# Kernel tuning notes

Hardware: AMD Instinct MI355X
Metric: run time of the kernel (lower is better)

The kernel has to match this reference:

```python
import jax, jax.numpy as jnp
import numpy as np
import math

D_MODEL = 512
N_HEADS = 8
MAX_SEQ_LEN = 4096
DENSITY = 0.3


def _make_random_mask(key, seq_len, density=DENSITY):
    # rand < density, symmetrized via (m + m.T)/2, clamped to [0,1], diag = 1
    u = jax.random.uniform(key, (seq_len, seq_len), dtype=jnp.float32)
    m = (u < density).astype(jnp.float32)
    m = jnp.clip((m + m.T) * 0.5, 0.0, 1.0)
    return m.at[jnp.diag_indices(seq_len)].set(1.0)


def setup_inputs() -> dict:
    key = jax.random.key(0)
    ks = jax.random.split(key, 10)
    B, T, C = 2, 4096, D_MODEL
    scale = 1.0 / math.sqrt(C)
    x = jax.random.normal(ks[0], (B, T, C), dtype=jnp.float32)
    mask = _make_random_mask(ks[1], MAX_SEQ_LEN)[:T, :T]
    # Linear weights stored as (in, out): y = x @ W + b
    Wq = jax.random.normal(ks[2], (C, C), dtype=jnp.float32) * scale
    Wk = jax.random.normal(ks[3], (C, C), dtype=jnp.float32) * scale
    Wv = jax.random.normal(ks[4], (C, C), dtype=jnp.float32) * scale
    Wo = jax.random.normal(ks[5], (C, C), dtype=jnp.float32) * scale
    bq = jax.random.normal(ks[6], (C,), dtype=jnp.float32) * scale
    bk = jax.random.normal(ks[7], (C,), dtype=jnp.float32) * scale
    bv = jax.random.normal(ks[8], (C,), dtype=jnp.float32) * scale
    bo = jax.random.normal(ks[9], (C,), dtype=jnp.float32) * scale
    return {"x": x, "mask": mask, "Wq": Wq, "bq": bq, "Wk": Wk, "bk": bk,
            "Wv": Wv, "bv": bv, "Wo": Wo, "bo": bo}


def reference(x, mask, Wq, bq, Wk, bk, Wv, bv, Wo, bo):
    B, T, C = x.shape
    H = N_HEADS
    dk = C // H
    q = (x @ Wq + bq).reshape(B, T, H, dk)
    k = (x @ Wk + bk).reshape(B, T, H, dk)
    v = (x @ Wv + bv).reshape(B, T, H, dk)
    # scores: [B, H, T, T]
    attn = jnp.einsum('bthd,bshd->bhts', q, k) / math.sqrt(dk)
    attn = attn * mask[None, None, :, :]  # multiplicative mask PRE-softmax
    p = jax.nn.softmax(attn, axis=-1)
    out = jnp.einsum('bhts,bshd->bthd', p, v).reshape(B, T, C)
    return out @ Wo + bo
```

## Files before the change

kernel.cpp:

```cpp
#include <hip/hip_runtime.h>
#include <math.h>

#define D_MODEL 512
#define N_HEADS 8
#define DK 64
#define QSCALE (0.0625f * 1.44269504089f)

typedef __attribute__((ext_vector_type(8))) short short8;
typedef __attribute__((ext_vector_type(4))) float f32x4;
typedef __attribute__((ext_vector_type(16))) float f32x16;

typedef __attribute__((address_space(1))) const unsigned as1_uint;
typedef __attribute__((address_space(3))) unsigned as3_uint;

__device__ __forceinline__ unsigned short f2bf(float f) {
    unsigned u = __builtin_bit_cast(unsigned, f);
    u = (u + 0x7fff + ((u >> 16) & 1)) >> 16;
    return (unsigned short)u;
}

__global__ __launch_bounds__(256) void cvt_x_kernel(const float* __restrict__ x,
                                                    unsigned short* __restrict__ xb, int n8)
{
    int i = blockIdx.x * 256 + threadIdx.x;
    if (i >= n8) return;
    float4 a = ((const float4*)x)[i * 2];
    float4 b = ((const float4*)x)[i * 2 + 1];
    short8 o;
    o[0] = f2bf(a.x); o[1] = f2bf(a.y); o[2] = f2bf(a.z); o[3] = f2bf(a.w);
    o[4] = f2bf(b.x); o[5] = f2bf(b.y); o[6] = f2bf(b.z); o[7] = f2bf(b.w);
    ((short8*)xb)[i] = o;
}

__global__ __launch_bounds__(256) void cvt_mask_kernel(const float* __restrict__ m,
                                                       unsigned char* __restrict__ mu, int n4)
{
    int i = blockIdx.x * 256 + threadIdx.x;
    if (i >= n4) return;
    float4 v = ((const float4*)m)[i];
    uchar4 o = { (unsigned char)(v.x * 2.0f + 0.5f),
                 (unsigned char)(v.y * 2.0f + 0.5f),
                 (unsigned char)(v.z * 2.0f + 0.5f),
                 (unsigned char)(v.w * 2.0f + 0.5f) };
    ((uchar4*)mu)[i] = o;
}

__global__ __launch_bounds__(256) void cvt_wt_kernel(const float* __restrict__ W,
                                                     unsigned short* __restrict__ Wt)
{
    __shared__ float tile[64][65];
    int t = threadIdx.x;
    int c0 = blockIdx.x * 64;
    int r0 = blockIdx.y * 64;
    #pragma unroll
    for (int i = 0; i < 16; i++) {
        int e = i * 256 + t, r = e >> 6, c = e & 63;
        tile[c][r] = W[(size_t)(r0 + r) * D_MODEL + c0 + c];
    }
    __syncthreads();
    #pragma unroll
    for (int i = 0; i < 16; i++) {
        int e = i * 256 + t, n = e >> 6, kk = e & 63;
        Wt[(size_t)(c0 + n) * D_MODEL + r0 + kk] = f2bf(tile[n][kk]);
    }
}

__global__ __launch_bounds__(512) void gemm_qkv_kernel(
    const unsigned short* __restrict__ A, const unsigned short* __restrict__ Wt,
    const float* __restrict__ bq, const float* __restrict__ bk, const float* __restrict__ bv,
    unsigned short* __restrict__ qb, unsigned short* __restrict__ kb,
    unsigned short* __restrict__ vb, int M, int T)
{
    constexpr int K = D_MODEL;
    __shared__ unsigned short As[2][128 * 32];
    __shared__ unsigned short Bs[2][128 * 32];
    int t = threadIdx.x;
    int lane = t & 63, w = t >> 6;
    int ql = lane & 15, kg = lane >> 4;
    int m0 = blockIdx.y * 128, n0 = blockIdx.x * 128;
    int wm = w >> 2, wn = w & 3;
    bool vmode = (n0 >= 1024);

    const unsigned short* srcA = A + (size_t)(m0 + (t >> 2)) * K + (t & 3) * 8;
    const unsigned short* srcB = Wt + (size_t)(n0 + (t >> 2)) * K + (t & 3) * 8;

    f32x4 acc[4][2];
    #pragma unroll
    for (int i = 0; i < 4; i++)
        #pragma unroll
        for (int j = 0; j < 2; j++) { f32x4 z = {0.f, 0.f, 0.f, 0.f}; acc[i][j] = z; }

    constexpr int NIT = K / 32;
    int cur = 0;
    __builtin_amdgcn_global_load_lds((as1_uint*)(srcA),
        (as3_uint*)((char*)&As[0][0] + w * 1024), 16, 0, 0);
    __builtin_amdgcn_global_load_lds((as1_uint*)(srcB),
        (as3_uint*)((char*)&Bs[0][0] + w * 1024), 16, 0, 0);
    __syncthreads();

    for (int it = 0; it < NIT; ++it) {
        if (it + 1 < NIT) {
            int k0 = (it + 1) * 32;
            __builtin_amdgcn_global_load_lds((as1_uint*)(srcA + k0),
                (as3_uint*)((char*)&As[cur ^ 1][0] + w * 1024), 16, 0, 0);
            __builtin_amdgcn_global_load_lds((as1_uint*)(srcB + k0),
                (as3_uint*)((char*)&Bs[cur ^ 1][0] + w * 1024), 16, 0, 0);
        }
        short8 af[4], bfr[2];
        #pragma unroll
        for (int fm = 0; fm < 4; fm++)
            af[fm] = *(const short8*)((const char*)&As[cur][0] + (wm * 64 + fm * 16 + ql) * 64 + kg * 16);
        #pragma unroll
        for (int fn = 0; fn < 2; fn++)
            bfr[fn] = *(const short8*)((const char*)&Bs[cur][0] + (wn * 32 + fn * 16 + ql) * 64 + kg * 16);
        if (vmode) {
            #pragma unroll
            for (int fm = 0; fm < 4; fm++)
                #pragma unroll
                for (int fn = 0; fn < 2; fn++)
                    acc[fm][fn] = __builtin_amdgcn_mfma_f32_16x16x32_bf16(bfr[fn], af[fm], acc[fm][fn], 0, 0, 0);
        } else {
            #pragma unroll
            for (int fm = 0; fm < 4; fm++)
                #pragma unroll
                for (int fn = 0; fn < 2; fn++)
                    acc[fm][fn] = __builtin_amdgcn_mfma_f32_16x16x32_bf16(af[fm], bfr[fn], acc[fm][fn], 0, 0, 0);
        }
        __syncthreads();
        cur ^= 1;
    }

    #pragma unroll
    for (int fm = 0; fm < 4; fm++) {
        #pragma unroll
        for (int fn = 0; fn < 2; fn++) {
            if (vmode) {
                int m = m0 + wm * 64 + fm * 16 + ql;
                int b = m / T, tt = m % T;
                #pragma unroll
                for (int r = 0; r < 4; r++) {
                    int n = (n0 - 1024) + wn * 32 + fn * 16 + kg * 4 + r;
                    float val = acc[fm][fn][r] + bv[n];
                    int h = n >> 6, d = n & 63;
                    vb[((size_t)(b * N_HEADS + h) * DK + d) * T + tt] = f2bf(val);
                }
            } else {
                int n = n0 + wn * 32 + fn * 16 + ql;
                int nn = n & 511;
                bool isq = (n0 < 512);
                float bn = isq ? bq[nn] : bk[nn];
                unsigned short* dst = isq ? qb : kb;
                int h = nn >> 6, d = nn & 63;
                #pragma unroll
                for (int r = 0; r < 4; r++) {
                    int m = m0 + wm * 64 + fm * 16 + kg * 4 + r;
                    int b = m / T, tt = m % T;
                    float val = acc[fm][fn][r] + bn;
                    if (isq) val *= QSCALE;
                    dst[((size_t)(b * N_HEADS + h) * T + tt) * DK + d] = f2bf(val);
                }
            }
        }
    }
}

__global__ __launch_bounds__(512) void gemm_out_kernel(
    const unsigned short* __restrict__ A, const unsigned short* __restrict__ Bt,
    const float* __restrict__ bias, float* __restrict__ outp, int M)
{
    constexpr int K = D_MODEL;
    __shared__ unsigned short As[2][128 * 32];
    __shared__ unsigned short Bs[2][128 * 32];
    int t = threadIdx.x;
    int lane = t & 63, w = t >> 6;
    int ql = lane & 15, kg = lane >> 4;
    int m0 = blockIdx.y * 128, n0 = blockIdx.x * 128;
    int wm = w >> 2, wn = w & 3;

    const unsigned short* srcA = A + (size_t)(m0 + (t >> 2)) * K + (t & 3) * 8;
    const unsigned short* srcB = Bt + (size_t)(n0 + (t >> 2)) * K + (t & 3) * 8;

    f32x4 acc[4][2];
    #pragma unroll
    for (int i = 0; i < 4; i++)
        #pragma unroll
        for (int j = 0; j < 2; j++) { f32x4 z = {0.f, 0.f, 0.f, 0.f}; acc[i][j] = z; }

    constexpr int NIT = K / 32;
    int cur = 0;
    __builtin_amdgcn_global_load_lds((as1_uint*)(srcA),
        (as3_uint*)((char*)&As[0][0] + w * 1024), 16, 0, 0);
    __builtin_amdgcn_global_load_lds((as1_uint*)(srcB),
        (as3_uint*)((char*)&Bs[0][0] + w * 1024), 16, 0, 0);
    __syncthreads();

    for (int it = 0; it < NIT; ++it) {
        if (it + 1 < NIT) {
            int k0 = (it + 1) * 32;
            __builtin_amdgcn_global_load_lds((as1_uint*)(srcA + k0),
                (as3_uint*)((char*)&As[cur ^ 1][0] + w * 1024), 16, 0, 0);
            __builtin_amdgcn_global_load_lds((as1_uint*)(srcB + k0),
                (as3_uint*)((char*)&Bs[cur ^ 1][0] + w * 1024), 16, 0, 0);
        }
        short8 af[4], bfr[2];
        #pragma unroll
        for (int fm = 0; fm < 4; fm++)
            af[fm] = *(const short8*)((const char*)&As[cur][0] + (wm * 64 + fm * 16 + ql) * 64 + kg * 16);
        #pragma unroll
        for (int fn = 0; fn < 2; fn++)
            bfr[fn] = *(const short8*)((const char*)&Bs[cur][0] + (wn * 32 + fn * 16 + ql) * 64 + kg * 16);
        #pragma unroll
        for (int fm = 0; fm < 4; fm++)
            #pragma unroll
            for (int fn = 0; fn < 2; fn++)
                acc[fm][fn] = __builtin_amdgcn_mfma_f32_16x16x32_bf16(af[fm], bfr[fn], acc[fm][fn], 0, 0, 0);
        __syncthreads();
        cur ^= 1;
    }

    #pragma unroll
    for (int fm = 0; fm < 4; fm++) {
        #pragma unroll
        for (int fn = 0; fn < 2; fn++) {
            int n = n0 + wn * 32 + fn * 16 + ql;
            float bn = bias[n];
            #pragma unroll
            for (int r = 0; r < 4; r++) {
                int m = m0 + wm * 64 + fm * 16 + kg * 4 + r;
                outp[(size_t)m * D_MODEL + n] = acc[fm][fn][r] + bn;
            }
        }
    }
}

__global__ __launch_bounds__(256) void attn_mfma_kernel(
    const unsigned short* __restrict__ q, const unsigned short* __restrict__ k,
    const unsigned short* __restrict__ v, const unsigned char* __restrict__ mu,
    unsigned short* __restrict__ out, int B, int T)
{
    __shared__ unsigned short Ks[2][64 * 64];
    __shared__ unsigned short Vt[2][64 * 64];

    int t = threadIdx.x;
    int lane = t & 63, w = t >> 6;
    int ln = lane & 31, hi = lane >> 5;
    int bh = blockIdx.x;
    int qt = blockIdx.y;
    int hh = bh & (N_HEADS - 1), b = bh >> 3;
    int qr0 = qt * 128;

    const char* kbase = (const char*)(k + (size_t)bh * T * DK);
    const char* vbase = (const char*)(v + (size_t)bh * DK * T);

    int lin0 = w * 1024 + lane * 16;
    int lin1 = 4096 + lin0;
    int row0 = lin0 >> 7, row1 = lin1 >> 7;
    int sw0 = (row0 & 7) << 4, sw1 = (row1 & 7) << 4;
    const char* gK0 = kbase + (lin0 ^ sw0);
    const char* gK1 = kbase + (lin1 ^ sw1);
    const char* gV0 = vbase + (size_t)row0 * (2 * T) + ((lin0 & 127) ^ sw0);
    const char* gV1 = vbase + (size_t)row1 * (2 * T) + ((lin1 & 127) ^ sw1);

    short8 qfr[4];
    {
        const unsigned short* qrow = q + ((size_t)bh * T + qr0 + w * 32 + ln) * DK + hi * 8;
        #pragma unroll
        for (int ks = 0; ks < 4; ks++)
            qfr[ks] = *(const short8*)(qrow + ks * 16);
    }

    const unsigned char* mbase = mu + (size_t)(qr0 + w * 32 + ln) * T + 4 * hi;

    f32x16 oacc[2];
    #pragma unroll
    for (int db = 0; db < 2; db++)
        #pragma unroll
        for (int i = 0; i < 16; i++) oacc[db][i] = 0.f;
    float lacc = 0.f;

    unsigned mcur[8];
    #pragma unroll
    for (int rb = 0; rb < 2; rb++)
        #pragma unroll
        for (int g = 0; g < 4; g++)
            mcur[rb * 4 + g] = *(const unsigned*)(mbase + rb * 32 + g * 8);
    __builtin_amdgcn_global_load_lds((as1_uint*)gK0, (as3_uint*)((char*)&Ks[0][0] + lin0), 16, 0, 0);
    __builtin_amdgcn_global_load_lds((as1_uint*)gK1, (as3_uint*)((char*)&Ks[0][0] + lin1), 16, 0, 0);
    __builtin_amdgcn_global_load_lds((as1_uint*)gV0, (as3_uint*)((char*)&Vt[0][0] + lin0), 16, 0, 0);
    __builtin_amdgcn_global_load_lds((as1_uint*)gV1, (as3_uint*)((char*)&Vt[0][0] + lin1), 16, 0, 0);

    int ntiles = T / 64;
    for (int kt = 0; kt < ntiles; kt++) {
        __syncthreads();
        int cur = kt & 1;
        bool havenext = (kt + 1) < ntiles;

        unsigned mnxt[8];
        if (havenext) {
            const unsigned char* mp = mbase + (size_t)(kt + 1) * 64;
            #pragma unroll
            for (int rb = 0; rb < 2; rb++)
                #pragma unroll
                for (int g = 0; g < 4; g++)
                    mnxt[rb * 4 + g] = *(const unsigned*)(mp + rb * 32 + g * 8);
            size_t ko = (size_t)(kt + 1) * 8192;
            size_t vo = (size_t)(kt + 1) * 128;
            __builtin_amdgcn_global_load_lds((as1_uint*)(gK0 + ko),
                (as3_uint*)((char*)&Ks[cur ^ 1][0] + lin0), 16, 0, 0);
            __builtin_amdgcn_global_load_lds((as1_uint*)(gK1 + ko),
                (as3_uint*)((char*)&Ks[cur ^ 1][0] + lin1), 16, 0, 0);
            __builtin_amdgcn_global_load_lds((as1_uint*)(gV0 + vo),
                (as3_uint*)((char*)&Vt[cur ^ 1][0] + lin0), 16, 0, 0);
            __builtin_amdgcn_global_load_lds((as1_uint*)(gV1 + vo),
                (as3_uint*)((char*)&Vt[cur ^ 1][0] + lin1), 16, 0, 0);
        }

        f32x16 sacc[2];
        #pragma unroll
        for (int rb = 0; rb < 2; rb++)
            #pragma unroll
            for (int i = 0; i < 16; i++) sacc[rb][i] = 0.f;
        __builtin_amdgcn_s_setprio(1);
        #pragma unroll
        for (int ks = 0; ks < 4; ks++) {
            #pragma unroll
            for (int rb = 0; rb < 2; rb++) {
                int row = rb * 32 + ln;
                short8 kf = *(const short8*)((const char*)&Ks[cur][0] +
                            ((row * 128 + ks * 32 + hi * 16) ^ ((row & 7) << 4)));
                sacc[rb] = __builtin_amdgcn_mfma_f32_32x32x16_bf16(kf, qfr[ks], sacc[rb], 0, 0, 0);
            }
        }
        __builtin_amdgcn_s_setprio(0);

        short8 pa[4];
        #pragma unroll
        for (int rb = 0; rb < 2; rb++) {
            float p[16];
            #pragma unroll
            for (int g = 0; g < 4; g++) {
                unsigned mw = mcur[rb * 4 + g];
                float p0 = __builtin_amdgcn_exp2f(sacc[rb][g * 4 + 0] * (float)(mw & 0xffu));
                float p1 = __builtin_amdgcn_exp2f(sacc[rb][g * 4 + 1] * (float)((mw >> 8) & 0xffu));
                float p2 = __builtin_amdgcn_exp2f(sacc[rb][g * 4 + 2] * (float)((mw >> 16) & 0xffu));
                float p3 = __builtin_amdgcn_exp2f(sacc[rb][g * 4 + 3] * (float)(mw >> 24));
                p[g * 4 + 0] = p0; p[g * 4 + 1] = p1; p[g * 4 + 2] = p2; p[g * 4 + 3] = p3;
                lacc += (p0 + p1) + (p2 + p3);
            }
            #pragma unroll
            for (int kl = 0; kl < 2; kl++) {
                int b0 = kl * 8;
                unsigned d0, d1, d2, d3;
                asm("v_cvt_pk_bf16_f32 %0, %1, %2" : "=v"(d0) : "v"(p[b0 + 0]), "v"(p[b0 + 1]));
                asm("v_cvt_pk_bf16_f32 %0, %1, %2" : "=v"(d1) : "v"(p[b0 + 2]), "v"(p[b0 + 3]));
                asm("v_cvt_pk_bf16_f32 %0, %1, %2" : "=v"(d2) : "v"(p[b0 + 4]), "v"(p[b0 + 5]));
                asm("v_cvt_pk_bf16_f32 %0, %1, %2" : "=v"(d3) : "v"(p[b0 + 6]), "v"(p[b0 + 7]));
                asm("v_permlane32_swap_b32 %0, %1" : "+v"(d0), "+v"(d2));
                asm("v_permlane32_swap_b32 %0, %1" : "+v"(d1), "+v"(d3));
                uint4 fr = { d0, d1, d2, d3 };
                pa[rb * 2 + kl] = __builtin_bit_cast(short8, fr);
            }
        }

        __builtin_amdgcn_s_setprio(1);
        #pragma unroll
        for (int ks = 0; ks < 4; ks++) {
            #pragma unroll
            for (int db = 0; db < 2; db++) {
                int row = db * 32 + ln;
                short8 vb = *(const short8*)((const char*)&Vt[cur][0] +
                            ((row * 128 + ks * 32 + hi * 16) ^ ((row & 7) << 4)));
                oacc[db] = __builtin_amdgcn_mfma_f32_32x32x16_bf16(pa[ks], vb, oacc[db], 0, 0, 0);
            }
        }
        __builtin_amdgcn_s_setprio(0);

        if (havenext) {
            #pragma unroll
            for (int c = 0; c < 8; c++) mcur[c] = mnxt[c];
        }
    }

    lacc += __shfl_xor(lacc, 32, 64);

    #pragma unroll
    for (int reg = 0; reg < 16; reg++) {
        int qoff = (reg & 3) + 8 * (reg >> 2) + 4 * hi;
        float linv = 1.0f / __shfl(lacc, qoff, 64);
        size_t rowo = ((size_t)b * T + qr0 + w * 32 + qoff) * D_MODEL + hh * DK + ln;
        out[rowo]      = f2bf(oacc[0][reg] * linv);
        out[rowo + 32] = f2bf(oacc[1][reg] * linv);
    }
}

extern "C" void kernel_launch(void* const* d_in, const int* in_sizes, int n_in,
                              void* d_out, int out_size, void* d_ws, size_t ws_size,
                              hipStream_t stream) {
    const float* x    = (const float*)d_in[0];
    const float* mask = (const float*)d_in[1];
    const float* Wq   = (const float*)d_in[2];
    const float* bq   = (const float*)d_in[3];
    const float* Wk   = (const float*)d_in[4];
    const float* bk   = (const float*)d_in[5];
    const float* Wv   = (const float*)d_in[6];
    const float* bv   = (const float*)d_in[7];
    const float* Wo   = (const float*)d_in[8];
    const float* bo   = (const float*)d_in[9];

    int T = (int)(sqrt((double)in_sizes[1]) + 0.5);
    int C = D_MODEL;
    int B = in_sizes[0] / (T * C);
    int M = B * T;

    size_t MK = (size_t)M * C;
    unsigned short* xb  = (unsigned short*)d_ws;
    unsigned short* Wtq = xb + MK;
    unsigned short* Wtk = Wtq + (size_t)C * C;
    unsigned short* Wtv = Wtk + (size_t)C * C;
    unsigned short* Wto = Wtv + (size_t)C * C;
    unsigned short* qb  = Wto + (size_t)C * C;
    unsigned short* kb  = qb + MK;
    unsigned short* vb  = kb + MK;
    unsigned short* attb = vb + MK;
    unsigned char*  mu  = (unsigned char*)(attb + MK);

    int n8 = (int)(MK / 8);
    cvt_x_kernel<<<(n8 + 255) / 256, 256, 0, stream>>>(x, xb, n8);
    int n4 = T * T / 4;
    cvt_mask_kernel<<<(n4 + 255) / 256, 256, 0, stream>>>(mask, mu, n4);
    dim3 wtg(C / 64, C / 64, 1);
    cvt_wt_kernel<<<wtg, 256, 0, stream>>>(Wq, Wtq);
    cvt_wt_kernel<<<wtg, 256, 0, stream>>>(Wk, Wtk);
    cvt_wt_kernel<<<wtg, 256, 0, stream>>>(Wv, Wtv);
    cvt_wt_kernel<<<wtg, 256, 0, stream>>>(Wo, Wto);

    dim3 gq(3 * C / 128, M / 128, 1);
    gemm_qkv_kernel<<<gq, 512, 0, stream>>>(xb, Wtq, bq, bk, bv, qb, kb, vb, M, T);

    dim3 ga(B * N_HEADS, T / 128, 1);
    attn_mfma_kernel<<<ga, 256, 0, stream>>>(qb, kb, vb, mu, attb, B, T);

    dim3 gg(C / 128, M / 128, 1);
    gemm_out_kernel<<<gg, 512, 0, stream>>>(attb, Wto, bo, (float*)d_out, M);
}
```

Before: 220.9 us.

## Process two KV tiles per barrier in attention and batch weight conversions

The attention loop now stages two 64-key K/V tiles per double-buffer slot, so each __syncthreads and prefetch round covers 128 keys, halving the barrier count and deepening the prefetch. It also merges the four weight-transpose launches into one kernel with a z-dimension. LDS use doubles to 64KB per block and mask registers double, which may lower occupancy.

```diff
diff --git a/kernel.cpp b/kernel.cpp
--- a/kernel.cpp
+++ b/kernel.cpp
@@ -45,10 +45,15 @@
     ((uchar4*)mu)[i] = o;
 }
 
-__global__ __launch_bounds__(256) void cvt_wt_kernel(const float* __restrict__ W,
-                                                     unsigned short* __restrict__ Wt)
+__global__ __launch_bounds__(256) void cvt_wt4_kernel(
+    const float* __restrict__ Wq, const float* __restrict__ Wk,
+    const float* __restrict__ Wv, const float* __restrict__ Wo,
+    unsigned short* __restrict__ Wt)
 {
     __shared__ float tile[64][65];
+    int z = blockIdx.z;
+    const float* W = (z == 0) ? Wq : (z == 1) ? Wk : (z == 2) ? Wv : Wo;
+    unsigned short* dst = Wt + (size_t)z * D_MODEL * D_MODEL;
     int t = threadIdx.x;
     int c0 = blockIdx.x * 64;
     int r0 = blockIdx.y * 64;
@@ -61,7 +66,7 @@
     #pragma unroll
     for (int i = 0; i < 16; i++) {
         int e = i * 256 + t, n = e >> 6, kk = e & 63;
-        Wt[(size_t)(c0 + n) * D_MODEL + r0 + kk] = f2bf(tile[n][kk]);
+        dst[(size_t)(c0 + n) * D_MODEL + r0 + kk] = f2bf(tile[n][kk]);
     }
 }
 
@@ -238,8 +243,8 @@
     const unsigned short* __restrict__ v, const unsigned char* __restrict__ mu,
     unsigned short* __restrict__ out, int B, int T)
 {
-    __shared__ unsigned short Ks[2][64 * 64];
-    __shared__ unsigned short Vt[2][64 * 64];
+    __shared__ unsigned short Ks[2][2][64 * 64];
+    __shared__ unsigned short Vt[2][2][64 * 64];
 
     int t = threadIdx.x;
     int lane = t & 63, w = t >> 6;
@@ -278,106 +283,126 @@
         for (int i = 0; i < 16; i++) oacc[db][i] = 0.f;
     float lacc = 0.f;
 
-    unsigned mcur[8];
-    #pragma unroll
-    for (int rb = 0; rb < 2; rb++)
-        #pragma unroll
-        for (int g = 0; g < 4; g++)
-            mcur[rb * 4 + g] = *(const unsigned*)(mbase + rb * 32 + g * 8);
-    __builtin_amdgcn_global_load_lds((as1_uint*)gK0, (as3_uint*)((char*)&Ks[0][0] + lin0), 16, 0, 0);
-    __builtin_amdgcn_global_load_lds((as1_uint*)gK1, (as3_uint*)((char*)&Ks[0][0] + lin1), 16, 0, 0);
-    __builtin_amdgcn_global_load_lds((as1_uint*)gV0, (as3_uint*)((char*)&Vt[0][0] + lin0), 16, 0, 0);
-    __builtin_amdgcn_global_load_lds((as1_uint*)gV1, (as3_uint*)((char*)&Vt[0][0] + lin1), 16, 0, 0);
-
-    int ntiles = T / 64;
-    for (int kt = 0; kt < ntiles; kt++) {
+    unsigned mcur[2][8];
+    #pragma unroll
+    for (int s = 0; s < 2; s++)
+        #pragma unroll
+        for (int rb = 0; rb < 2; rb++)
+            #pragma unroll
+            for (int g = 0; g < 4; g++)
+                mcur[s][rb * 4 + g] = *(const unsigned*)(mbase + s * 64 + rb * 32 + g * 8);
+    #pragma unroll
+    for (int s = 0; s < 2; s++) {
+        __builtin_amdgcn_global_load_lds((as1_uint*)(gK0 + (size_t)s * 8192),
+            (as3_uint*)((char*)&Ks[0][s][0] + lin0), 16, 0, 0);
+        __builtin_amdgcn_global_load_lds((as1_uint*)(gK1 + (size_t)s * 8192),
+            (as3_uint*)((char*)&Ks[0][s][0] + lin1), 16, 0, 0);
+        __builtin_amdgcn_global_load_lds((as1_uint*)(gV0 + (size_t)s * 128),
+            (as3_uint*)((char*)&Vt[0][s][0] + lin0), 16, 0, 0);
+        __builtin_amdgcn_global_load_lds((as1_uint*)(gV1 + (size_t)s * 128),
+            (as3_uint*)((char*)&Vt[0][s][0] + lin1), 16, 0, 0);
+    }
+
+    int npairs = T / 128;
+    for (int j = 0; j < npairs; j++) {
         __syncthreads();
-        int cur = kt & 1;
-        bool havenext = (kt + 1) < ntiles;
-
-        unsigned mnxt[8];
+        int cur = j & 1;
+        bool havenext = (j + 1) < npairs;
+
+        unsigned mnxt[2][8];
         if (havenext) {
-            const unsigned char* mp = mbase + (size_t)(kt + 1) * 64;
+            #pragma unroll
+            for (int s = 0; s < 2; s++) {
+                const unsigned char* mp = mbase + (size_t)(2 * (j + 1) + s) * 64;
+                #pragma unroll
+                for (int rb = 0; rb < 2; rb++)
+                    #pragma unroll
+                    for (int g = 0; g < 4; g++)
+                        mnxt[s][rb * 4 + g] = *(const unsigned*)(mp + rb * 32 + g * 8);
+            }
+            size_t ko = (size_t)(2 * (j + 1)) * 8192;
+            size_t vo = (size_t)(2 * (j + 1)) * 128;
+            #pragma unroll
+            for (int s = 0; s < 2; s++) {
+                __builtin_amdgcn_global_load_lds((as1_uint*)(gK0 + ko + (size_t)s * 8192),
+                    (as3_uint*)((char*)&Ks[cur ^ 1][s][0] + lin0), 16, 0, 0);
+                __builtin_amdgcn_global_load_lds((as1_uint*)(gK1 + ko + (size_t)s * 8192),
+                    (as3_uint*)((char*)&Ks[cur ^ 1][s][0] + lin1), 16, 0, 0);
+                __builtin_amdgcn_global_load_lds((as1_uint*)(gV0 + vo + (size_t)s * 128),
+                    (as3_uint*)((char*)&Vt[cur ^ 1][s][0] + lin0), 16, 0, 0);
+                __builtin_amdgcn_global_load_lds((as1_uint*)(gV1 + vo + (size_t)s * 128),
+                    (as3_uint*)((char*)&Vt[cur ^ 1][s][0] + lin1), 16, 0, 0);
+            }
+        }
+
+        #pragma unroll
+        for (int s = 0; s < 2; s++) {
+            f32x16 sacc[2];
             #pragma unroll
             for (int rb = 0; rb < 2; rb++)
                 #pragma unroll
-                for (int g = 0; g < 4; g++)
-                    mnxt[rb * 4 + g] = *(const unsigned*)(mp + rb * 32 + g * 8);
-            size_t ko = (size_t)(kt + 1) * 8192;
-            size_t vo = (size_t)(kt + 1) * 128;
-            __builtin_amdgcn_global_load_lds((as1_uint*)(gK0 + ko),
-                (as3_uint*)((char*)&Ks[cur ^ 1][0] + lin0), 16, 0, 0);
-            __builtin_amdgcn_global_load_lds((as1_uint*)(gK1 + ko),
-                (as3_uint*)((char*)&Ks[cur ^ 1][0] + lin1), 16, 0, 0);
-            __builtin_amdgcn_global_load_lds((as1_uint*)(gV0 + vo),
-                (as3_uint*)((char*)&Vt[cur ^ 1][0] + lin0), 16, 0, 0);
-            __builtin_amdgcn_global_load_lds((as1_uint*)(gV1 + vo),
-                (as3_uint*)((char*)&Vt[cur ^ 1][0] + lin1), 16, 0, 0);
-        }
-
-        f32x16 sacc[2];
-        #pragma unroll
-        for (int rb = 0; rb < 2; rb++)
-            #pragma unroll
-            for (int i = 0; i < 16; i++) sacc[rb][i] = 0.f;
-        __builtin_amdgcn_s_setprio(1);
-        #pragma unroll
-        for (int ks = 0; ks < 4; ks++) {
+                for (int i = 0; i < 16; i++) sacc[rb][i] = 0.f;
+            __builtin_amdgcn_s_setprio(1);
+            #pragma unroll
+            for (int ks = 0; ks < 4; ks++) {
+                #pragma unroll
+                for (int rb = 0; rb < 2; rb++) {
+                    int row = rb * 32 + ln;
+                    short8 kf = *(const short8*)((const char*)&Ks[cur][s][0] +
+                                ((row * 128 + ks * 32 + hi * 16) ^ ((row & 7) << 4)));
+                    sacc[rb] = __builtin_amdgcn_mfma_f32_32x32x16_bf16(kf, qfr[ks], sacc[rb], 0, 0, 0);
+                }
+            }
+            __builtin_amdgcn_s_setprio(0);
+
+            short8 pa[4];
             #pragma unroll
             for (int rb = 0; rb < 2; rb++) {
-                int row = rb * 32 + ln;
-                short8 kf = *(const short8*)((const char*)&Ks[cur][0] +
-                            ((row * 128 + ks * 32 + hi * 16) ^ ((row & 7) << 4)));
-                sacc[rb] = __builtin_amdgcn_mfma_f32_32x32x16_bf16(kf, qfr[ks], sacc[rb], 0, 0, 0);
-            }
-        }
-        __builtin_amdgcn_s_setprio(0);
-
-        short8 pa[4];
-        #pragma unroll
-        for (int rb = 0; rb < 2; rb++) {
-            float p[16];
-            #pragma unroll
-            for (int g = 0; g < 4; g++) {
-                unsigned mw = mcur[rb * 4 + g];
-                float p0 = __builtin_amdgcn_exp2f(sacc[rb][g * 4 + 0] * (float)(mw & 0xffu));
-                float p1 = __builtin_amdgcn_exp2f(sacc[rb][g * 4 + 1] * (float)((mw >> 8) & 0xffu));
-                float p2 = __builtin_amdgcn_exp2f(sacc[rb][g * 4 + 2] * (float)((mw >> 16) & 0xffu));
-                float p3 = __builtin_amdgcn_exp2f(sacc[rb][g * 4 + 3] * (float)(mw >> 24));
-                p[g * 4 + 0] = p0; p[g * 4 + 1] = p1; p[g * 4 + 2] = p2; p[g * 4 + 3] = p3;
-                lacc += (p0 + p1) + (p2 + p3);
-            }
-            #pragma unroll
-            for (int kl = 0; kl < 2; kl++) {
-                int b0 = kl * 8;
-                unsigned d0, d1, d2, d3;
-                asm("v_cvt_pk_bf16_f32 %0, %1, %2" : "=v"(d0) : "v"(p[b0 + 0]), "v"(p[b0 + 1]));
-                asm("v_cvt_pk_bf16_f32 %0, %1, %2" : "=v"(d1) : "v"(p[b0 + 2]), "v"(p[b0 + 3]));
-                asm("v_cvt_pk_bf16_f32 %0, %1, %2" : "=v"(d2) : "v"(p[b0 + 4]), "v"(p[b0 + 5]));
-                asm("v_cvt_pk_bf16_f32 %0, %1, %2" : "=v"(d3) : "v"(p[b0 + 6]), "v"(p[b0 + 7]));
-                asm("v_permlane32_swap_b32 %0, %1" : "+v"(d0), "+v"(d2));
-                asm("v_permlane32_swap_b32 %0, %1" : "+v"(d1), "+v"(d3));
-                uint4 fr = { d0, d1, d2, d3 };
-                pa[rb * 2 + kl] = __builtin_bit_cast(short8, fr);
-            }
-        }
-
-        __builtin_amdgcn_s_setprio(1);
-        #pragma unroll
-        for (int ks = 0; ks < 4; ks++) {
-            #pragma unroll
-            for (int db = 0; db < 2; db++) {
-                int row = db * 32 + ln;
-                short8 vb = *(const short8*)((const char*)&Vt[cur][0] +
-                            ((row * 128 + ks * 32 + hi * 16) ^ ((row & 7) << 4)));
-                oacc[db] = __builtin_amdgcn_mfma_f32_32x32x16_bf16(pa[ks], vb, oacc[db], 0, 0, 0);
-            }
-        }
-        __builtin_amdgcn_s_setprio(0);
+                float p[16];
+                #pragma unroll
+                for (int g = 0; g < 4; g++) {
+                    unsigned mw = mcur[s][rb * 4 + g];
+                    float p0 = __builtin_amdgcn_exp2f(sacc[rb][g * 4 + 0] * (float)(mw & 0xffu));
+                    float p1 = __builtin_amdgcn_exp2f(sacc[rb][g * 4 + 1] * (float)((mw >> 8) & 0xffu));
+                    float p2 = __builtin_amdgcn_exp2f(sacc[rb][g * 4 + 2] * (float)((mw >> 16) & 0xffu));
+                    float p3 = __builtin_amdgcn_exp2f(sacc[rb][g * 4 + 3] * (float)(mw >> 24));
+                    p[g * 4 + 0] = p0; p[g * 4 + 1] = p1; p[g * 4 + 2] = p2; p[g * 4 + 3] = p3;
+                    lacc += (p0 + p1) + (p2 + p3);
+                }
+                #pragma unroll
+                for (int kl = 0; kl < 2; kl++) {
+                    int b0 = kl * 8;
+                    unsigned d0, d1, d2, d3;
+                    asm("v_cvt_pk_bf16_f32 %0, %1, %2" : "=v"(d0) : "v"(p[b0 + 0]), "v"(p[b0 + 1]));
+                    asm("v_cvt_pk_bf16_f32 %0, %1, %2" : "=v"(d1) : "v"(p[b0 + 2]), "v"(p[b0 + 3]));
+                    asm("v_cvt_pk_bf16_f32 %0, %1, %2" : "=v"(d2) : "v"(p[b0 + 4]), "v"(p[b0 + 5]));
+                    asm("v_cvt_pk_bf16_f32 %0, %1, %2" : "=v"(d3) : "v"(p[b0 + 6]), "v"(p[b0 + 7]));
+                    asm("v_permlane32_swap_b32 %0, %1" : "+v"(d0), "+v"(d2));
+                    asm("v_permlane32_swap_b32 %0, %1" : "+v"(d1), "+v"(d3));
+                    uint4 fr = { d0, d1, d2, d3 };
+                    pa[rb * 2 + kl] = __builtin_bit_cast(short8, fr);
+                }
+            }
+
+            __builtin_amdgcn_s_setprio(1);
+            #pragma unroll
+            for (int ks = 0; ks < 4; ks++) {
+                #pragma unroll
+                for (int db = 0; db < 2; db++) {
+                    int row = db * 32 + ln;
+                    short8 vb = *(const short8*)((const char*)&Vt[cur][s][0] +
+                                ((row * 128 + ks * 32 + hi * 16) ^ ((row & 7) << 4)));
+                    oacc[db] = __builtin_amdgcn_mfma_f32_32x32x16_bf16(pa[ks], vb, oacc[db], 0, 0, 0);
+                }
+            }
+            __builtin_amdgcn_s_setprio(0);
+        }
 
         if (havenext) {
             #pragma unroll
-            for (int c = 0; c < 8; c++) mcur[c] = mnxt[c];
+            for (int s = 0; s < 2; s++)
+                #pragma unroll
+                for (int c = 0; c < 8; c++) mcur[s][c] = mnxt[s][c];
         }
     }
 
@@ -415,10 +440,8 @@
     size_t MK = (size_t)M * C;
     unsigned short* xb  = (unsigned short*)d_ws;
     unsigned short* Wtq = xb + MK;
-    unsigned short* Wtk = Wtq + (size_t)C * C;
-    unsigned short* Wtv = Wtk + (size_t)C * C;
-    unsigned short* Wto = Wtv + (size_t)C * C;
-    unsigned short* qb  = Wto + (size_t)C * C;
+    unsigned short* Wto = Wtq + 3 * (size_t)C * C;
+    unsigned short* qb  = Wtq + 4 * (size_t)C * C;
     unsigned short* kb  = qb + MK;
     unsigned short* vb  = kb + MK;
     unsigned short* attb = vb + MK;
@@ -428,11 +451,8 @@
     cvt_x_kernel<<<(n8 + 255) / 256, 256, 0, stream>>>(x, xb, n8);
     int n4 = T * T / 4;
     cvt_mask_kernel<<<(n4 + 255) / 256, 256, 0, stream>>>(mask, mu, n4);
-    dim3 wtg(C / 64, C / 64, 1);
-    cvt_wt_kernel<<<wtg, 256, 0, stream>>>(Wq, Wtq);
-    cvt_wt_kernel<<<wtg, 256, 0, stream>>>(Wk, Wtk);
-    cvt_wt_kernel<<<wtg, 256, 0, stream>>>(Wv, Wtv);
-    cvt_wt_kernel<<<wtg, 256, 0, stream>>>(Wo, Wto);
+    dim3 wtg(C / 64, C / 64, 4);
+    cvt_wt4_kernel<<<wtg, 256, 0, stream>>>(Wq, Wk, Wv, Wo, Wtq);
 
     dim3 gq(3 * C / 128, M / 128, 1);
     gemm_qkv_kernel<<<gq, 512, 0, stream>>>(xb, Wtq, bq, bk, bv, qb, kb, vb, M, T);
```

Measured after the change: 217.2 us. About the same (-1.7%).

## Split attention key range across two wave groups and merge partial sums in LDS

Applied to the files above, without the earlier changes.

The attention block grows to 512 threads, and two groups of four waves each process half of the key sequence for the same 128 query rows. Each group has its own double-buffered K/V tiles. Their partial outputs and row sums are reduced through shared memory at the end. Because the kernel skips the running max, the partials can be added directly with no rescaling. The aim is more waves in flight for latency hiding within the same grid of 256 blocks. It also drops the mask prefetch into registers, which may expose mask load latency. The four weight-convert launches are merged into one launch using blockIdx.z.

```diff
diff --git a/kernel.cpp b/kernel.cpp
--- a/kernel.cpp
+++ b/kernel.cpp
@@ -45,10 +45,15 @@
     ((uchar4*)mu)[i] = o;
 }
 
-__global__ __launch_bounds__(256) void cvt_wt_kernel(const float* __restrict__ W,
-                                                     unsigned short* __restrict__ Wt)
+__global__ __launch_bounds__(256) void cvt_wt4_kernel(
+    const float* __restrict__ Wq, const float* __restrict__ Wk,
+    const float* __restrict__ Wv, const float* __restrict__ Wo,
+    unsigned short* __restrict__ Wt)
 {
     __shared__ float tile[64][65];
+    int z = blockIdx.z;
+    const float* W = (z == 0) ? Wq : (z == 1) ? Wk : (z == 2) ? Wv : Wo;
+    unsigned short* dst = Wt + (size_t)z * D_MODEL * D_MODEL;
     int t = threadIdx.x;
     int c0 = blockIdx.x * 64;
     int r0 = blockIdx.y * 64;
@@ -61,7 +66,7 @@
     #pragma unroll
     for (int i = 0; i < 16; i++) {
         int e = i * 256 + t, n = e >> 6, kk = e & 63;
-        Wt[(size_t)(c0 + n) * D_MODEL + r0 + kk] = f2bf(tile[n][kk]);
+        dst[(size_t)(c0 + n) * D_MODEL + r0 + kk] = f2bf(tile[n][kk]);
     }
 }
 
@@ -233,43 +238,46 @@
     }
 }
 
-__global__ __launch_bounds__(256) void attn_mfma_kernel(
+__global__ __launch_bounds__(512, 4) void attn_mfma_kernel(
     const unsigned short* __restrict__ q, const unsigned short* __restrict__ k,
     const unsigned short* __restrict__ v, const unsigned char* __restrict__ mu,
     unsigned short* __restrict__ out, int B, int T)
 {
-    __shared__ unsigned short Ks[2][64 * 64];
-    __shared__ unsigned short Vt[2][64 * 64];
+    __shared__ unsigned short Ks[2][2][64 * 64];
+    __shared__ unsigned short Vt[2][2][64 * 64];
 
     int t = threadIdx.x;
     int lane = t & 63, w = t >> 6;
+    int wg = w & 3, g = w >> 2;
     int ln = lane & 31, hi = lane >> 5;
     int bh = blockIdx.x;
     int qt = blockIdx.y;
     int hh = bh & (N_HEADS - 1), b = bh >> 3;
     int qr0 = qt * 128;
-
-    const char* kbase = (const char*)(k + (size_t)bh * T * DK);
+    int Th = T >> 1;
+
+    const char* kbase = (const char*)(k + (size_t)bh * T * DK) + (size_t)g * Th * 128;
     const char* vbase = (const char*)(v + (size_t)bh * DK * T);
-
-    int lin0 = w * 1024 + lane * 16;
+    size_t gvofs = (size_t)g * Th * 2;
+
+    int lin0 = wg * 1024 + lane * 16;
     int lin1 = 4096 + lin0;
     int row0 = lin0 >> 7, row1 = lin1 >> 7;
     int sw0 = (row0 & 7) << 4, sw1 = (row1 & 7) << 4;
     const char* gK0 = kbase + (lin0 ^ sw0);
     const char* gK1 = kbase + (lin1 ^ sw1);
-    const char* gV0 = vbase + (size_t)row0 * (2 * T) + ((lin0 & 127) ^ sw0);
-    const char* gV1 = vbase + (size_t)row1 * (2 * T) + ((lin1 & 127) ^ sw1);
+    const char* gV0 = vbase + (size_t)row0 * (2 * T) + gvofs + ((lin0 & 127) ^ sw0);
+    const char* gV1 = vbase + (size_t)row1 * (2 * T) + gvofs + ((lin1 & 127) ^ sw1);
 
     short8 qfr[4];
     {
-        const unsigned short* qrow = q + ((size_t)bh * T + qr0 + w * 32 + ln) * DK + hi * 8;
+        const unsigned short* qrow = q + ((size_t)bh * T + qr0 + wg * 32 + ln) * DK + hi * 8;
         #pragma unroll
         for (int ks = 0; ks < 4; ks++)
             qfr[ks] = *(const short8*)(qrow + ks * 16);
     }
 
-    const unsigned char* mbase = mu + (size_t)(qr0 + w * 32 + ln) * T + 4 * hi;
+    const unsigned char* mbase = mu + (size_t)(qr0 + wg * 32 + ln) * T + (size_t)g * Th + 4 * hi;
 
     f32x16 oacc[2];
     #pragma unroll
@@ -278,41 +286,37 @@
         for (int i = 0; i < 16; i++) oacc[db][i] = 0.f;
     float lacc = 0.f;
 
-    unsigned mcur[8];
-    #pragma unroll
-    for (int rb = 0; rb < 2; rb++)
-        #pragma unroll
-        for (int g = 0; g < 4; g++)
-            mcur[rb * 4 + g] = *(const unsigned*)(mbase + rb * 32 + g * 8);
-    __builtin_amdgcn_global_load_lds((as1_uint*)gK0, (as3_uint*)((char*)&Ks[0][0] + lin0), 16, 0, 0);
-    __builtin_amdgcn_global_load_lds((as1_uint*)gK1, (as3_uint*)((char*)&Ks[0][0] + lin1), 16, 0, 0);
-    __builtin_amdgcn_global_load_lds((as1_uint*)gV0, (as3_uint*)((char*)&Vt[0][0] + lin0), 16, 0, 0);
-    __builtin_amdgcn_global_load_lds((as1_uint*)gV1, (as3_uint*)((char*)&Vt[0][0] + lin1), 16, 0, 0);
-
-    int ntiles = T / 64;
+    __builtin_amdgcn_global_load_lds((as1_uint*)gK0, (as3_uint*)((char*)&Ks[g][0][0] + lin0), 16, 0, 0);
+    __builtin_amdgcn_global_load_lds((as1_uint*)gK1, (as3_uint*)((char*)&Ks[g][0][0] + lin1), 16, 0, 0);
+    __builtin_amdgcn_global_load_lds((as1_uint*)gV0, (as3_uint*)((char*)&Vt[g][0][0] + lin0), 16, 0, 0);
+    __builtin_amdgcn_global_load_lds((as1_uint*)gV1, (as3_uint*)((char*)&Vt[g][0][0] + lin1), 16, 0, 0);
+
+    int ntiles = Th / 64;
     for (int kt = 0; kt < ntiles; kt++) {
         __syncthreads();
         int cur = kt & 1;
-        bool havenext = (kt + 1) < ntiles;
-
-        unsigned mnxt[8];
-        if (havenext) {
-            const unsigned char* mp = mbase + (size_t)(kt + 1) * 64;
+
+        unsigned mcur[8];
+        {
+            const unsigned char* mp = mbase + (size_t)kt * 64;
             #pragma unroll
             for (int rb = 0; rb < 2; rb++)
                 #pragma unroll
-                for (int g = 0; g < 4; g++)
-                    mnxt[rb * 4 + g] = *(const unsigned*)(mp + rb * 32 + g * 8);
+                for (int gg = 0; gg < 4; gg++)
+                    mcur[rb * 4 + gg] = *(const unsigned*)(mp + rb * 32 + gg * 8);
+        }
+
+        if (kt + 1 < ntiles) {
             size_t ko = (size_t)(kt + 1) * 8192;
             size_t vo = (size_t)(kt + 1) * 128;
             __builtin_amdgcn_global_load_lds((as1_uint*)(gK0 + ko),
-                (as3_uint*)((char*)&Ks[cur ^ 1][0] + lin0), 16, 0, 0);
+                (as3_uint*)((char*)&Ks[g][cur ^ 1][0] + lin0), 16, 0, 0);
             __builtin_amdgcn_global_load_lds((as1_uint*)(gK1 + ko),
-                (as3_uint*)((char*)&Ks[cur ^ 1][0] + lin1), 16, 0, 0);
+                (as3_uint*)((char*)&Ks[g][cur ^ 1][0] + lin1), 16, 0, 0);
             __builtin_amdgcn_global_load_lds((as1_uint*)(gV0 + vo),
-                (as3_uint*)((char*)&Vt[cur ^ 1][0] + lin0), 16, 0, 0);
+                (as3_uint*)((char*)&Vt[g][cur ^ 1][0] + lin0), 16, 0, 0);
             __builtin_amdgcn_global_load_lds((as1_uint*)(gV1 + vo),
-                (as3_uint*)((char*)&Vt[cur ^ 1][0] + lin1), 16, 0, 0);
+                (as3_uint*)((char*)&Vt[g][cur ^ 1][0] + lin1), 16, 0, 0);
         }
 
         f32x16 sacc[2];
@@ -326,7 +330,7 @@
             #pragma unroll
             for (int rb = 0; rb < 2; rb++) {
                 int row = rb * 32 + ln;
-                short8 kf = *(const short8*)((const char*)&Ks[cur][0] +
+                short8 kf = *(const short8*)((const char*)&Ks[g][cur][0] +
                             ((row * 128 + ks * 32 + hi * 16) ^ ((row & 7) << 4)));
                 sacc[rb] = __builtin_amdgcn_mfma_f32_32x32x16_bf16(kf, qfr[ks], sacc[rb], 0, 0, 0);
             }
@@ -338,13 +342,13 @@
         for (int rb = 0; rb < 2; rb++) {
             float p[16];
             #pragma unroll
-            for (int g = 0; g < 4; g++) {
-                unsigned mw = mcur[rb * 4 + g];
-                float p0 = __builtin_amdgcn_exp2f(sacc[rb][g * 4 + 0] * (float)(mw & 0xffu));
-                float p1 = __builtin_amdgcn_exp2f(sacc[rb][g * 4 + 1] * (float)((mw >> 8) & 0xffu));
-                float p2 = __builtin_amdgcn_exp2f(sacc[rb][g * 4 + 2] * (float)((mw >> 16) & 0xffu));
-                float p3 = __builtin_amdgcn_exp2f(sacc[rb][g * 4 + 3] * (float)(mw >> 24));
-                p[g * 4 + 0] = p0; p[g * 4 + 1] = p1; p[g * 4 + 2] = p2; p[g * 4 + 3] = p3;
+            for (int gg = 0; gg < 4; gg++) {
+                unsigned mw = mcur[rb * 4 + gg];
+                float p0 = __builtin_amdgcn_exp2f(sacc[rb][gg * 4 + 0] * (float)(mw & 0xffu));
+                float p1 = __builtin_amdgcn_exp2f(sacc[rb][gg * 4 + 1] * (float)((mw >> 8) & 0xffu));
+                float p2 = __builtin_amdgcn_exp2f(sacc[rb][gg * 4 + 2] * (float)((mw >> 16) & 0xffu));
+                float p3 = __builtin_amdgcn_exp2f(sacc[rb][gg * 4 + 3] * (float)(mw >> 24));
+                p[gg * 4 + 0] = p0; p[gg * 4 + 1] = p1; p[gg * 4 + 2] = p2; p[gg * 4 + 3] = p3;
                 lacc += (p0 + p1) + (p2 + p3);
             }
             #pragma unroll
@@ -368,28 +372,41 @@
             #pragma unroll
             for (int db = 0; db < 2; db++) {
                 int row = db * 32 + ln;
-                short8 vb = *(const short8*)((const char*)&Vt[cur][0] +
+                short8 vb = *(const short8*)((const char*)&Vt[g][cur][0] +
                             ((row * 128 + ks * 32 + hi * 16) ^ ((row & 7) << 4)));
                 oacc[db] = __builtin_amdgcn_mfma_f32_32x32x16_bf16(pa[ks], vb, oacc[db], 0, 0, 0);
             }
         }
         __builtin_amdgcn_s_setprio(0);
-
-        if (havenext) {
-            #pragma unroll
-            for (int c = 0; c < 8; c++) mcur[c] = mnxt[c];
-        }
     }
 
     lacc += __shfl_xor(lacc, 32, 64);
 
-    #pragma unroll
-    for (int reg = 0; reg < 16; reg++) {
-        int qoff = (reg & 3) + 8 * (reg >> 2) + 4 * hi;
-        float linv = 1.0f / __shfl(lacc, qoff, 64);
-        size_t rowo = ((size_t)b * T + qr0 + w * 32 + qoff) * D_MODEL + hh * DK + ln;
-        out[rowo]      = f2bf(oacc[0][reg] * linv);
-        out[rowo + 32] = f2bf(oacc[1][reg] * linv);
+    __syncthreads();
+    float* Ls = (float*)&Ks[0][0][0];
+    float* Ll = (float*)&Vt[0][0][0];
+    int sidx = wg * 64 + lane;
+    if (g == 1) {
+        #pragma unroll
+        for (int reg = 0; reg < 16; reg++) {
+            Ls[reg * 256 + sidx]        = oacc[0][reg];
+            Ls[(16 + reg) * 256 + sidx] = oacc[1][reg];
+        }
+        Ll[sidx] = lacc;
+    }
+    __syncthreads();
+    if (g == 0) {
+        float lsum = lacc + Ll[sidx];
+        #pragma unroll
+        for (int reg = 0; reg < 16; reg++) {
+            float o0 = oacc[0][reg] + Ls[reg * 256 + sidx];
+            float o1 = oacc[1][reg] + Ls[(16 + reg) * 256 + sidx];
+            int qoff = (reg & 3) + 8 * (reg >> 2) + 4 * hi;
+            float linv = 1.0f / __shfl(lsum, qoff, 64);
+            size_t rowo = ((size_t)b * T + qr0 + wg * 32 + qoff) * D_MODEL + hh * DK + ln;
+            out[rowo]      = f2bf(o0 * linv);
+            out[rowo + 32] = f2bf(o1 * linv);
+        }
     }
 }
 
@@ -415,10 +432,8 @@
     size_t MK = (size_t)M * C;
     unsigned short* xb  = (unsigned short*)d_ws;
     unsigned short* Wtq = xb + MK;
-    unsigned short* Wtk = Wtq + (size_t)C * C;
-    unsigned short* Wtv = Wtk + (size_t)C * C;
-    unsigned short* Wto = Wtv + (size_t)C * C;
-    unsigned short* qb  = Wto + (size_t)C * C;
+    unsigned short* Wto = Wtq + 3 * (size_t)C * C;
+    unsigned short* qb  = Wtq + 4 * (size_t)C * C;
     unsigned short* kb  = qb + MK;
     unsigned short* vb  = kb + MK;
     unsigned short* attb = vb + MK;
@@ -428,17 +443,14 @@
     cvt_x_kernel<<<(n8 + 255) / 256, 256, 0, stream>>>(x, xb, n8);
     int n4 = T * T / 4;
     cvt_mask_kernel<<<(n4 + 255) / 256, 256, 0, stream>>>(mask, mu, n4);
-    dim3 wtg(C / 64, C / 64, 1);
-    cvt_wt_kernel<<<wtg, 256, 0, stream>>>(Wq, Wtq);
-    cvt_wt_kernel<<<wtg, 256, 0, stream>>>(Wk, Wtk);
-    cvt_wt_kernel<<<wtg, 256, 0, stream>>>(Wv, Wtv);
-    cvt_wt_kernel<<<wtg, 256, 0, stream>>>(Wo, Wto);
+    dim3 wtg(C / 64, C / 64, 4);
+    cvt_wt4_kernel<<<wtg, 256, 0, stream>>>(Wq, Wk, Wv, Wo, Wtq);
 
     dim3 gq(3 * C / 128, M / 128, 1);
     gemm_qkv_kernel<<<gq, 512, 0, stream>>>(xb, Wtq, bq, bk, bv, qb, kb, vb, M, T);
 
     dim3 ga(B * N_HEADS, T / 128, 1);
-    attn_mfma_kernel<<<ga, 256, 0, stream>>>(qb, kb, vb, mu, attb, B, T);
+    attn_mfma_kernel<<<ga, 512, 0, stream>>>(qb, kb, vb, mu, attb, B, T);
 
     dim3 gg(C / 128, M / 128, 1);
     gemm_out_kernel<<<gg, 512, 0, stream>>>(attb, Wto, bo, (float*)d_out, M);
```

Result: slower. 229.9 us (+4.1%).

## Merge weight conversion launches and remap attention blocks for XCD L2 locality

Applied to the files above, without the earlier changes.

The four weight-transpose/convert launches become one launch that uses blockIdx.z to pick the matrix. The attention grid is flattened to 1D, and for the B=2, T=4096 shape the block index is remapped so each XCD (chosen round-robin by n&7) handles two whole (batch, head) pairs. That way the K/V tiles for a head stay in a single XCD's L2. The aim is fewer launch overheads and fewer cross-XCD L2 misses on K/V, at the cost of a hardcoded special-case mapping.

```diff
diff --git a/kernel.cpp b/kernel.cpp
--- a/kernel.cpp
+++ b/kernel.cpp
@@ -45,10 +45,15 @@
     ((uchar4*)mu)[i] = o;
 }
 
-__global__ __launch_bounds__(256) void cvt_wt_kernel(const float* __restrict__ W,
-                                                     unsigned short* __restrict__ Wt)
+__global__ __launch_bounds__(256) void cvt_wt4_kernel(
+    const float* __restrict__ Wq, const float* __restrict__ Wk,
+    const float* __restrict__ Wv, const float* __restrict__ Wo,
+    unsigned short* __restrict__ Wt)
 {
     __shared__ float tile[64][65];
+    int z = blockIdx.z;
+    const float* W = (z == 0) ? Wq : (z == 1) ? Wk : (z == 2) ? Wv : Wo;
+    unsigned short* dst = Wt + (size_t)z * D_MODEL * D_MODEL;
     int t = threadIdx.x;
     int c0 = blockIdx.x * 64;
     int r0 = blockIdx.y * 64;
@@ -61,7 +66,7 @@
     #pragma unroll
     for (int i = 0; i < 16; i++) {
         int e = i * 256 + t, n = e >> 6, kk = e & 63;
-        Wt[(size_t)(c0 + n) * D_MODEL + r0 + kk] = f2bf(tile[n][kk]);
+        dst[(size_t)(c0 + n) * D_MODEL + r0 + kk] = f2bf(tile[n][kk]);
     }
 }
 
@@ -244,8 +249,19 @@
     int t = threadIdx.x;
     int lane = t & 63, w = t >> 6;
     int ln = lane & 31, hi = lane >> 5;
-    int bh = blockIdx.x;
-    int qt = blockIdx.y;
+
+    int n = blockIdx.x;
+    int nbh = B * N_HEADS;
+    int nqt = T / 128;
+    int bh, qt;
+    if (nbh == 16 && nqt == 32) {
+        int xcd = n & 7, s = n >> 3;
+        bh = xcd * 2 + (s >> 5);
+        qt = s & 31;
+    } else {
+        bh = n / nqt;
+        qt = n % nqt;
+    }
     int hh = bh & (N_HEADS - 1), b = bh >> 3;
     int qr0 = qt * 128;
 
@@ -415,10 +431,8 @@
     size_t MK = (size_t)M * C;
     unsigned short* xb  = (unsigned short*)d_ws;
     unsigned short* Wtq = xb + MK;
-    unsigned short* Wtk = Wtq + (size_t)C * C;
-    unsigned short* Wtv = Wtk + (size_t)C * C;
-    unsigned short* Wto = Wtv + (size_t)C * C;
-    unsigned short* qb  = Wto + (size_t)C * C;
+    unsigned short* Wto = Wtq + 3 * (size_t)C * C;
+    unsigned short* qb  = Wtq + 4 * (size_t)C * C;
     unsigned short* kb  = qb + MK;
     unsigned short* vb  = kb + MK;
     unsigned short* attb = vb + MK;
@@ -428,17 +442,14 @@
     cvt_x_kernel<<<(n8 + 255) / 256, 256, 0, stream>>>(x, xb, n8);
     int n4 = T * T / 4;
     cvt_mask_kernel<<<(n4 + 255) / 256, 256, 0, stream>>>(mask, mu, n4);
-    dim3 wtg(C / 64, C / 64, 1);
-    cvt_wt_kernel<<<wtg, 256, 0, stream>>>(Wq, Wtq);
-    cvt_wt_kernel<<<wtg, 256, 0, stream>>>(Wk, Wtk);
-    cvt_wt_kernel<<<wtg, 256, 0, stream>>>(Wv, Wtv);
-    cvt_wt_kernel<<<wtg, 256, 0, stream>>>(Wo, Wto);
+    dim3 wtg(C / 64, C / 64, 4);
+    cvt_wt4_kernel<<<wtg, 256, 0, stream>>>(Wq, Wk, Wv, Wo, Wtq);
 
     dim3 gq(3 * C / 128, M / 128, 1);
     gemm_qkv_kernel<<<gq, 512, 0, stream>>>(xb, Wtq, bq, bk, bv, qb, kb, vb, M, T);
 
-    dim3 ga(B * N_HEADS, T / 128, 1);
-    attn_mfma_kernel<<<ga, 256, 0, stream>>>(qb, kb, vb, mu, attb, B, T);
+    int nblocks = (B * N_HEADS) * (T / 128);
+    attn_mfma_kernel<<<nblocks, 256, 0, stream>>>(qb, kb, vb, mu, attb, B, T);
 
     dim3 gg(C / 128, M / 128, 1);
     gemm_out_kernel<<<gg, 512, 0, stream>>>(attb, Wto, bo, (float*)d_out, M);
```

Result: faster. 211.4 us (-4.3%).
